# Optimization experiments

Hardware: AMD Instinct MI355X
Metric: run time of the kernel (lower is better)

The kernel has to match this reference:

```python
import jax, jax.numpy as jnp
import numpy as np
from jax import lax

B, A, SEQ, FIN = 512, 16, 50, 6
H, H2, T, G, S = 256, 128, 60, 64, 6
GR0, GR1 = -50.0, 50.0
CELL = (GR1 - GR0) / G
NTYPES, EMB = 10, 16
NENC, NL = 5, 2

def setup_inputs() -> dict:
    key = jax.random.key(0)
    ks = jax.random.split(key, 40)
    def rn(k, shape, scale=0.05):
        return (jax.random.normal(k, shape) * scale).astype(jnp.float32)
    history = jax.random.normal(ks[0], (B, A, SEQ, FIN), dtype=jnp.float32)
    types = jax.random.randint(ks[1], (B,), 0, NTYPES)
    history = history.at[:, 0, 0, 5].set(types.astype(jnp.float32))
    d = dict(history=history)
    d['emb'] = rn(ks[2], (NTYPES, EMB))
    d['fe_W1'] = rn(ks[3], (FIN + EMB, H)); d['fe_b1'] = jnp.zeros((H,), jnp.float32)
    d['fe_W2'] = rn(ks[4], (H, H));        d['fe_b2'] = jnp.zeros((H,), jnp.float32)
    d['enc_Wih'] = rn(ks[5], (NENC, NL, H, 3 * H))
    d['enc_Whh'] = rn(ks[6], (NENC, NL, H, 3 * H))
    d['enc_bih'] = rn(ks[7], (NENC, NL, 3 * H))
    d['enc_bhh'] = rn(ks[8], (NENC, NL, 3 * H))
    d['dec_Wih0'] = rn(ks[9], (2, 3 * H)); d['dec_Whh0'] = rn(ks[10], (H, 3 * H))
    d['dec_bih0'] = rn(ks[11], (3 * H));   d['dec_bhh0'] = rn(ks[12], (3 * H))
    d['dec_Wih1'] = rn(ks[13], (H, 3 * H)); d['dec_Whh1'] = rn(ks[14], (H, 3 * H))
    d['dec_bih1'] = rn(ks[15], (3 * H));    d['dec_bhh1'] = rn(ks[16], (3 * H))
    d['hg_W1'] = rn(ks[17], (H, H));   d['hg_b1'] = jnp.zeros((H,), jnp.float32)
    d['hg_W2'] = rn(ks[18], (H, H2));  d['hg_b2'] = jnp.zeros((H2,), jnp.float32)
    d['hg_W3'] = rn(ks[19], (H2, T * 2)); d['hg_b3'] = jnp.zeros((T * 2,), jnp.float32)
    d['ce_W1'] = rn(ks[20], (H, H2));  d['ce_b1'] = jnp.zeros((H2,), jnp.float32)
    d['ce_W2'] = rn(ks[21], (H2, T));  d['ce_b2'] = jnp.zeros((T,), jnp.float32)
    d['hp_W1'] = rn(ks[22], (H, H));   d['hp_b1'] = jnp.zeros((H,), jnp.float32)
    d['hp_W2'] = rn(ks[23], (H, G * G)); d['hp_b2'] = jnp.zeros((G * G,), jnp.float32)
    return d

def _gru_cell(xt, h, Wih, Whh, bih, bhh):
    # torch GRU gate order: r, z, n
    gi = xt @ Wih + bih
    gh = h @ Whh + bhh
    Hd = h.shape[-1]
    r = jax.nn.sigmoid(gi[:, :Hd] + gh[:, :Hd])
    z = jax.nn.sigmoid(gi[:, Hd:2 * Hd] + gh[:, Hd:2 * Hd])
    n = jnp.tanh(gi[:, 2 * Hd:] + r * gh[:, 2 * Hd:])
    return (1.0 - z) * n + z * h

def _forward(history, emb, fe_W1, fe_b1, fe_W2, fe_b2,
             enc_Wih, enc_Whh, enc_bih, enc_bhh,
             dec_Wih0, dec_Whh0, dec_bih0, dec_bhh0,
             dec_Wih1, dec_Whh1, dec_bih1, dec_bhh1,
             hg_W1, hg_b1, hg_W2, hg_b2, hg_W3, hg_b3,
             ce_W1, ce_b1, ce_W2, ce_b2, hp_W1, hp_b1, hp_W2, hp_b2):
    ego = history[:, 0]                                   # [B,SEQ,6]
    etype = jnp.clip(ego[:, 0, 5].astype(jnp.int32), 0, 9)
    # type -> encoder index (vehicle,pedestrian,cyclist,bus,default)
    eidx = jnp.array([0, 1, 4, 2, 3, 4, 4, 4, 4, 4], jnp.int32)[etype]
    te = emb[etype]                                       # [B,16]
    x_in = jnp.concatenate([ego, jnp.broadcast_to(te[:, None, :], (B, SEQ, EMB))], axis=-1)
    feat = jax.nn.relu(x_in @ fe_W1 + fe_b1) @ fe_W2 + fe_b2  # [B,SEQ,H]

    # 2-layer GRU with per-example (type-gathered) weights
    x_cur = feat.transpose(1, 0, 2)                       # [SEQ,B,H]
    h_finals = []
    for l in range(NL):
        Wih = enc_Wih[eidx, l]; Whh = enc_Whh[eidx, l]    # [B,H,3H]
        bih = enc_bih[eidx, l]; bhh = enc_bhh[eidx, l]    # [B,3H]
        def step(h, xt, Wih=Wih, Whh=Whh, bih=bih, bhh=bhh):
            gi = jnp.einsum('bd,bdg->bg', xt, Wih) + bih
            gh = jnp.einsum('bh,bhg->bg', h, Whh) + bhh
            r = jax.nn.sigmoid(gi[:, :H] + gh[:, :H])
            z = jax.nn.sigmoid(gi[:, H:2 * H] + gh[:, H:2 * H])
            n = jnp.tanh(gi[:, 2 * H:] + r * gh[:, 2 * H:])
            hn = (1.0 - z) * n + z * h
            return hn, hn
        h_last, ys = lax.scan(step, jnp.zeros((B, H), feat.dtype), x_cur)
        x_cur = ys
        h_finals.append(h_last)
    enc_h0, enc_h1 = h_finals

    # decoder GRU, single timestep: x = last ego position
    x0 = ego[:, -1, :2]
    h0 = _gru_cell(x0, enc_h0, dec_Wih0, dec_Whh0, dec_bih0, dec_bhh0)
    h1 = _gru_cell(h0, enc_h1, dec_Wih1, dec_Whh1, dec_bih1, dec_bhh1)
    last_hidden = h1                                      # [B,H]

    traj = (jax.nn.relu(jax.nn.relu(last_hidden @ hg_W1 + hg_b1) @ hg_W2 + hg_b2) @ hg_W3 + hg_b3)
    traj = traj.reshape(B, T, 2)
    conf = jax.nn.relu(last_hidden @ ce_W1 + ce_b1) @ ce_W2 + ce_b2   # [B,T]

    key = jax.random.key(42)
    k_noise, k_samp = jax.random.split(key)
    noise = jax.random.normal(k_noise, (T, B, H), last_hidden.dtype)
    scale = (0.1 * jnp.arange(T, dtype=last_hidden.dtype) / T)[:, None, None]
    th = last_hidden[None] + noise * scale                # [T,B,H]
    logits = jax.nn.relu(th @ hp_W1 + hp_b1) @ hp_W2 + hp_b2  # [T,B,G*G]

    # vectorized multinomial over (samples, timesteps, batch)
    idx = jax.random.categorical(k_samp, logits, shape=(S - 1, T, B))  # int [S-1,T,B]
    x_idx = (idx % G).astype(jnp.float32)
    y_idx = (idx // G).astype(jnp.float32)
    pts = jnp.stack([GR0 + x_idx * CELL + CELL / 2,
                     GR0 + y_idx * CELL + CELL / 2], axis=-1)  # [S-1,T,B,2]
    pts = pts.transpose(2, 0, 1, 3)                       # [B,S-1,T,2]

    predictions = jnp.concatenate([traj[:, None], pts], axis=1)  # [B,S,T,2]
    decay = jnp.float32(0.9) ** jnp.arange(S, dtype=jnp.float32)
    confidences = conf.mean(axis=1)[:, None] * decay[None, :]    # [B,S]
    return predictions, confidences

def reference(history, emb, fe_W1, fe_b1, fe_W2, fe_b2,
              enc_Wih, enc_Whh, enc_bih, enc_bhh,
              dec_Wih0, dec_Whh0, dec_bih0, dec_bhh0,
              dec_Wih1, dec_Whh1, dec_bih1, dec_bhh1,
              hg_W1, hg_b1, hg_W2, hg_b2, hg_W3, hg_b3,
              ce_W1, ce_b1, ce_W2, ce_b2, hp_W1, hp_b1, hp_W2, hp_b2):
    return _forward(history, emb, fe_W1, fe_b1, fe_W2, fe_b2,
                    enc_Wih, enc_Whh, enc_bih, enc_bhh,
                    dec_Wih0, dec_Whh0, dec_bih0, dec_bhh0,
                    dec_Wih1, dec_Whh1, dec_bih1, dec_bhh1,
                    hg_W1, hg_b1, hg_W2, hg_b2, hg_W3, hg_b3,
                    ce_W1, ce_b1, ce_W2, ce_b2, hp_W1, hp_b1, hp_W2, hp_b2)
```

## Files before the change

### kernel.cpp

```cpp
#include <hip/hip_runtime.h>
#include <stdint.h>
#include <math.h>

#define JAX_PARTITIONABLE 1

#define B_ 512
#define SEQ_ 50
#define H_ 256
#define H2_ 128
#define T_ 60
#define S_ 6
#define EMB_ 16
#define NL_ 2
#define TG_ 768
#define CAT_ 4096
#define GUMBEL_N 629145600u
#define NOISE_N 7864320u

typedef float f32x2 __attribute__((ext_vector_type(2)));

#define PKFMA_LO(acc, w, h) \
  asm("v_pk_fma_f32 %0, %1, %2, %0 op_sel:[0,0,0] op_sel_hi:[1,0,1]" : "+v"(acc) : "v"(w), "v"(h))
#define PKFMA_HI(acc, w, h) \
  asm("v_pk_fma_f32 %0, %1, %2, %0 op_sel:[0,1,0] op_sel_hi:[1,1,1]" : "+v"(acc) : "v"(w), "v"(h))

__host__ __device__ inline uint32_t rotl32(uint32_t x, int r) {
#if defined(__HIP_DEVICE_COMPILE__)
  return __builtin_amdgcn_alignbit(x, x, 32 - r);
#else
  return (x << r) | (x >> (32 - r));
#endif
}

__host__ __device__ inline void tf2x32(uint32_t k0, uint32_t k1, uint32_t x0, uint32_t x1,
                                       uint32_t& o0, uint32_t& o1) {
  uint32_t ks2 = k0 ^ k1 ^ 0x1BD11BDAu;
  x0 += k0; x1 += k1;
#define TFR(r) do { x0 += x1; x1 = rotl32(x1, r); x1 ^= x0; } while (0)
  TFR(13); TFR(15); TFR(26); TFR(6);
  x0 += k1; x1 += ks2 + 1u;
  TFR(17); TFR(29); TFR(16); TFR(24);
  x0 += ks2; x1 += k0 + 2u;
  TFR(13); TFR(15); TFR(26); TFR(6);
  x0 += k0; x1 += k1 + 3u;
  TFR(17); TFR(29); TFR(16); TFR(24);
  x0 += k1; x1 += ks2 + 4u;
  TFR(13); TFR(15); TFR(26); TFR(6);
  x0 += ks2; x1 += k0 + 5u;
#undef TFR
  o0 = x0; o1 = x1;
}

__device__ inline uint32_t jax_bits(uint32_t k0, uint32_t k1, uint32_t i, uint32_t n) {
#if JAX_PARTITIONABLE
  (void)n;
  uint32_t a, b;
  tf2x32(k0, k1, 0u, i, a, b);
  return a ^ b;
#else
  uint32_t half = n >> 1;
  uint32_t lo = (i < half) ? i : (i - half);
  uint32_t a, b;
  tf2x32(k0, k1, lo, lo + half, a, b);
  return (i < half) ? a : b;
#endif
}

__device__ inline float bits_to_f01(uint32_t bits) {
  return __uint_as_float((bits >> 9) | 0x3f800000u) - 1.0f;
}

__device__ inline float erfinv_f(float x) {
  double xd = (double)x;
  float w = (float)(-log((1.0 - xd) * (1.0 + xd)));
  float p;
  if (w < 5.0f) {
    w = __fadd_rn(w, -2.5f);
    p = 2.81022636e-08f;
    p = __fadd_rn(3.43273939e-07f, __fmul_rn(p, w));
    p = __fadd_rn(-3.5233877e-06f, __fmul_rn(p, w));
    p = __fadd_rn(-4.39150654e-06f, __fmul_rn(p, w));
    p = __fadd_rn(0.00021858087f, __fmul_rn(p, w));
    p = __fadd_rn(-0.00125372503f, __fmul_rn(p, w));
    p = __fadd_rn(-0.00417768164f, __fmul_rn(p, w));
    p = __fadd_rn(0.246640727f, __fmul_rn(p, w));
    p = __fadd_rn(1.50140941f, __fmul_rn(p, w));
  } else {
    w = __fadd_rn(__fsqrt_rn(w), -3.0f);
    p = -0.000200214257f;
    p = __fadd_rn(0.000100950558f, __fmul_rn(p, w));
    p = __fadd_rn(0.00134934322f, __fmul_rn(p, w));
    p = __fadd_rn(-0.00367342844f, __fmul_rn(p, w));
    p = __fadd_rn(0.00573950773f, __fmul_rn(p, w));
    p = __fadd_rn(-0.0076224613f, __fmul_rn(p, w));
    p = __fadd_rn(0.00943887047f, __fmul_rn(p, w));
    p = __fadd_rn(1.00167406f, __fmul_rn(p, w));
    p = __fadd_rn(2.83297682f, __fmul_rn(p, w));
  }
  return __fmul_rn(p, x);
}

__device__ inline float gumbel_f32(uint32_t bits) {
  float f = bits_to_f01(bits);
  float u = fmaxf(f, 1.17549435e-38f);
  float l1 = logf(u);
  return -logf(-l1);
}

__device__ inline uint32_t orderkey(float s) {
  uint32_t sb = __float_as_uint(s);
  return (sb & 0x80000000u) ? ~sb : (sb | 0x80000000u);
}

__global__ __launch_bounds__(512) void k_init(const float* __restrict__ hist,
                                              float* __restrict__ x0buf, int* __restrict__ ip) {
  int b = threadIdx.x;
  if (b < B_) {
    float tv = hist[b * 4800 + 5];
    int et = (int)tv;
    et = et < 0 ? 0 : (et > 9 ? 9 : et);
    const int mp[10] = {0, 1, 4, 2, 3, 4, 4, 4, 4, 4};
    ip[b] = et;
    ip[512 + b] = mp[et];
    x0buf[b * 2 + 0] = hist[b * 4800 + 49 * 6 + 0];
    x0buf[b * 2 + 1] = hist[b * 4800 + 49 * 6 + 1];
  }
  __syncthreads();
  if (b == 0) {
    int cnt[5] = {0, 0, 0, 0, 0};
    for (int i = 0; i < B_; i++) cnt[ip[512 + i]]++;
    int off[6];
    off[0] = 0;
    for (int e = 0; e < 5; e++) off[e + 1] = off[e] + cnt[e];
    int pos[5];
    for (int e = 0; e < 5; e++) pos[e] = off[e];
    for (int i = 0; i < B_; i++) { int e = ip[512 + i]; ip[1024 + pos[e]++] = i; }
    int* tbl = ip + 1536;
    int nrt = 0;
    for (int e = 0; e < 5; e++) {
      int n = cnt[e];
      for (int s = 0; s < n; s += 16) {
        tbl[1 + nrt] = e;
        tbl[37 + nrt] = off[e] + s;
        tbl[73 + nrt] = (n - s) < 16 ? (n - s) : 16;
        nrt++;
      }
    }
    tbl[0] = nrt;
  }
}

__global__ void k_zero(uint32_t* p, int n) {
  int i = blockIdx.x * blockDim.x + threadIdx.x;
  if (i < n) p[i] = 0u;
}

__global__ __launch_bounds__(256) void k_pack(const float* __restrict__ Wih,
                                              const float* __restrict__ Whh,
                                              float4* __restrict__ wp) {
  int i = blockIdx.x * 256 + threadIdx.x;
  if (i >= 20 * 65536) return;
  int cl = i & 31;
  int k  = (i >> 5) & 255;
  int cg = (i >> 13) & 7;
  int em = i >> 16;
  int m = em & 1;
  int el = em >> 1;
  int c = cg * 32 + cl;
  const float* W = (m ? Whh : Wih) + (size_t)el * H_ * TG_;
  float4 v;
  v.x = W[k * TG_ + c];
  v.y = W[k * TG_ + H_ + c];
  v.z = W[k * TG_ + 2 * H_ + c];
  v.w = 0.0f;
  wp[i] = v;
}

__global__ __launch_bounds__(256) void k_feat(const float* __restrict__ hist, const float* __restrict__ emb,
    const float* __restrict__ W1, const float* __restrict__ b1,
    const float* __restrict__ W2, const float* __restrict__ b2,
    const int* __restrict__ ip, float* __restrict__ featbuf) {
  __shared__ float xs[16][22];
  __shared__ float t1[16][H_];
  int row0 = blockIdx.x * 16;
  int tid = threadIdx.x;
  for (int idx = tid; idx < 16 * 22; idx += 256) {
    int r = idx / 22, c = idx % 22;
    int g = row0 + r;
    int b = g / SEQ_, s = g % SEQ_;
    xs[r][c] = (c < 6) ? hist[b * 4800 + s * 6 + c] : emb[ip[b] * EMB_ + (c - 6)];
  }
  __syncthreads();
  int j = tid;
  {
    double acc[16];
    for (int r = 0; r < 16; r++) acc[r] = 0.0;
    for (int k = 0; k < 22; k++) {
      double w = (double)W1[k * H_ + j];
      for (int r = 0; r < 16; r++) acc[r] += (double)xs[r][k] * w;
    }
    double bb = (double)b1[j];
    for (int r = 0; r < 16; r++) t1[r][j] = fmaxf((float)(acc[r] + bb), 0.0f);
  }
  __syncthreads();
  {
    double acc[16];
    for (int r = 0; r < 16; r++) acc[r] = 0.0;
    for (int k = 0; k < H_; k++) {
      double w = (double)W2[k * H_ + j];
      for (int r = 0; r < 16; r++) acc[r] += (double)t1[r][k] * w;
    }
    double bb = (double)b2[j];
    for (int r = 0; r < 16; r++) {
      float v = (float)(acc[r] + bb);
      int g = row0 + r;
      int b = g / SEQ_, s = g % SEQ_;
      featbuf[(size_t)s * (B_ * H_) + (size_t)b * H_ + j] = v;
    }
  }
}

#define KS_STAGE(dst, src)                                             \
  for (int idx = tid; idx < 16 * 64; idx += 512) {                     \
    int r = idx >> 6, c4 = idx & 63;                                   \
    int rr = (r < nr) ? r : 0;                                         \
    int b = order[start + rr];                                         \
    if (c4 == 0) rowb[r] = b;                                          \
    *(float4*)&dst[r][c4 * 4] = *(const float4*)&src[b * H_ + c4 * 4]; \
  }

#define KS_LOOP(src)                                                        \
  for (int k = k0; k < k0 + 128; k += 4) {                                  \
    float4 w0 = wp[(k + 0) * 32], w1 = wp[(k + 1) * 32];                    \
    float4 w2 = wp[(k + 2) * 32], w3 = wp[(k + 3) * 32];                    \
    float4 xa = *(const float4*)&src[rs][k];                                \
    float4 xb = *(const float4*)&src[rs + 8][k];                            \
    a0 += (double)xa.x * (double)w0.x; a1 += (double)xb.x * (double)w0.x;   \
    z0 += (double)xa.x * (double)w0.y; z1 += (double)xb.x * (double)w0.y;   \
    n0 += (double)xa.x * (double)w0.z; n1 += (double)xb.x * (double)w0.z;   \
    a0 += (double)xa.y * (double)w1.x; a1 += (double)xb.y * (double)w1.x;   \
    z0 += (double)xa.y * (double)w1.y; z1 += (double)xb.y * (double)w1.y;   \
    n0 += (double)xa.y * (double)w1.z; n1 += (double)xb.y * (double)w1.z;   \
    a0 += (double)xa.z * (double)w2.x; a1 += (double)xb.z * (double)w2.x;   \
    z0 += (double)xa.z * (double)w2.y; z1 += (double)xb.z * (double)w2.y;   \
    n0 += (double)xa.z * (double)w2.z; n1 += (double)xb.z * (double)w2.z;   \
    a0 += (double)xa.w * (double)w3.x; a1 += (double)xb.w * (double)w3.x;   \
    z0 += (double)xa.w * (double)w3.y; z1 += (double)xb.w * (double)w3.y;   \
    n0 += (double)xa.w * (double)w3.z; n1 += (double)xb.w * (double)w3.z;   \
  }

__device__ __forceinline__ void gi_block_ks(float (*xs)[H_], int* rowb,
    double (*part)[32][6],
    int rt, int cg, int tid,
    const float* __restrict__ x, float* __restrict__ gi_out,
    const float4* __restrict__ wpack, const float* __restrict__ bih_base,
    int layer, const int* __restrict__ ip) {
  const int* tbl = ip + 1536;
  const int* order = ip + 1024;
  int nrt = tbl[0];
  if (rt >= nrt) return;
  int e = tbl[1 + rt];
  int start = tbl[37 + rt];
  int nr = tbl[73 + rt];
  KS_STAGE(xs, x)
  __syncthreads();
  int j = tid & 31, rs = (tid >> 5) & 7, kh = tid >> 8;
  int c = cg * 32 + j;
  int el = e * NL_ + layer;
  const float4* wp = wpack + (((size_t)(el * 2 + 0) * 8 + cg) * 256) * 32 + j;
  int k0 = kh * 128;
  double a0 = 0, a1 = 0, z0 = 0, z1 = 0, n0 = 0, n1 = 0;
  KS_LOOP(xs)
  if (kh) {
    double* pp = &part[rs][j][0];
    pp[0] = a0; pp[1] = a1; pp[2] = z0; pp[3] = z1; pp[4] = n0; pp[5] = n1;
  }
  __syncthreads();
  if (!kh) {
    const double* pp = &part[rs][j][0];
    a0 += pp[0]; a1 += pp[1]; z0 += pp[2]; z1 += pp[3]; n0 += pp[4]; n1 += pp[5];
    int cr = c, cz = H_ + c, cn = 2 * H_ + c;
    const float* bih = bih_base + (size_t)el * TG_;
    double br = (double)bih[cr], bz = (double)bih[cz], bn = (double)bih[cn];
    for (int p = 0; p < 2; p++) {
      int r = rs + 8 * p;
      if (r >= nr) continue;
      int b = rowb[r];
      gi_out[b * TG_ + cr] = (float)((p ? a1 : a0) + br);
      gi_out[b * TG_ + cz] = (float)((p ? z1 : z0) + bz);
      gi_out[b * TG_ + cn] = (float)((p ? n1 : n0) + bn);
    }
  }
}

__device__ __forceinline__ void step_block_ks(float (*hs)[H_], int* rowb,
    double (*part)[32][6],
    int rt, int cg, int tid,
    const float* __restrict__ gi_in, const float* __restrict__ hin,
    float* __restrict__ hout, float* __restrict__ ys,
    const float4* __restrict__ wpack, const float* __restrict__ bhh_base,
    int layer, const int* __restrict__ ip) {
  const int* tbl = ip + 1536;
  const int* order = ip + 1024;
  int nrt = tbl[0];
  if (rt >= nrt) return;
  int e = tbl[1 + rt];
  int start = tbl[37 + rt];
  int nr = tbl[73 + rt];
  KS_STAGE(hs, hin)
  __syncthreads();
  int j = tid & 31, rs = (tid >> 5) & 7, kh = tid >> 8;
  int c = cg * 32 + j;
  int el = e * NL_ + layer;
  const float4* wp = wpack + (((size_t)(el * 2 + 1) * 8 + cg) * 256) * 32 + j;
  int k0 = kh * 128;
  double a0 = 0, a1 = 0, z0 = 0, z1 = 0, n0 = 0, n1 = 0;
  KS_LOOP(hs)
  if (kh) {
    double* pp = &part[rs][j][0];
    pp[0] = a0; pp[1] = a1; pp[2] = z0; pp[3] = z1; pp[4] = n0; pp[5] = n1;
  }
  __syncthreads();
  if (!kh) {
    const double* pp = &part[rs][j][0];
    a0 += pp[0]; a1 += pp[1]; z0 += pp[2]; z1 += pp[3]; n0 += pp[4]; n1 += pp[5];
    int cr = c, cz = H_ + c, cn = 2 * H_ + c;
    const float* bhh = bhh_base + (size_t)el * TG_;
    double bhr = (double)bhh[cr], bhz = (double)bhh[cz], bhn = (double)bhh[cn];
    for (int p = 0; p < 2; p++) {
      int r = rs + 8 * p;
      if (r >= nr) continue;
      int b = rowb[r];
      double gir = (double)gi_in[b * TG_ + cr];
      double giz = (double)gi_in[b * TG_ + cz];
      double gin = (double)gi_in[b * TG_ + cn];
      double ghr = (p ? a1 : a0) + bhr;
      double ghz = (p ? z1 : z0) + bhz;
      double ghn = (p ? n1 : n0) + bhn;
      double rr = 1.0 / (1.0 + exp(-(gir + ghr)));
      double zz = 1.0 / (1.0 + exp(-(giz + ghz)));
      double nn = tanh(gin + rr * ghn);
      double hv = (double)hs[r][c];
      float hnew = (float)((1.0 - zz) * nn + zz * hv);
      hout[b * H_ + c] = hnew;
      if (ys) ys[b * H_ + c] = hnew;
    }
  }
}

__global__ __launch_bounds__(512) void k_pipe512(int d,
    const float* __restrict__ feat, float* __restrict__ ys0,
    float* __restrict__ gi0, float* __restrict__ gi1,
    float* __restrict__ h0A, float* __restrict__ h0B,
    float* __restrict__ h1A, float* __restrict__ h1B,
    const float4* __restrict__ wpack,
    const float* __restrict__ bih, const float* __restrict__ bhh,
    const int* __restrict__ ip) {
  __shared__ float sb[16][H_];
  __shared__ double part[8][32][6];
  __shared__ int rowb[16];
  int g = blockIdx.x;
  int grp = g / 288, bx = g % 288;
  int rt = bx >> 3, cg = bx & 7;
  int tid = threadIdx.x;
  if (grp == 0) {
    int t = d; if (t >= SEQ_) return;
    gi_block_ks(sb, rowb, part, rt, cg, tid, feat + (size_t)t * 131072,
                gi0 + (size_t)(t & 1) * 393216, wpack, bih, 0, ip);
  } else if (grp == 1) {
    int t = d - 1; if (t < 0 || t >= SEQ_) return;
    const float* hin = (t & 1) ? h0B : h0A;
    float* hout = (t & 1) ? h0A : h0B;
    step_block_ks(sb, rowb, part, rt, cg, tid, gi0 + (size_t)(t & 1) * 393216,
                  hin, hout, ys0 + (size_t)t * 131072, wpack, bhh, 0, ip);
  } else if (grp == 2) {
    int t = d - 2; if (t < 0 || t >= SEQ_) return;
    gi_block_ks(sb, rowb, part, rt, cg, tid, ys0 + (size_t)t * 131072,
                gi1 + (size_t)(t & 1) * 393216, wpack, bih, 1, ip);
  } else {
    int t = d - 3; if (t < 0 || t >= SEQ_) return;
    const float* hin = (t & 1) ? h1B : h1A;
    float* hout = (t & 1) ? h1A : h1B;
    step_block_ks(sb, rowb, part, rt, cg, tid, gi1 + (size_t)(t & 1) * 393216,
                  hin, hout, nullptr, wpack, bhh, 1, ip);
  }
}

__device__ __forceinline__ void gi_block_u(float (*xs)[H_], int* rowb,
    int rt, int cg, int tid,
    const float* __restrict__ x, float* __restrict__ gi_out,
    const float* __restrict__ Wih_base, const float* __restrict__ bih_base,
    int layer, const int* __restrict__ ip) {
  const int* tbl = ip + 1536;
  const int* order = ip + 1024;
  int nrt = tbl[0];
  if (rt >= nrt) return;
  int e = tbl[1 + rt];
  int start = tbl[37 + rt];
  int nr = tbl[73 + rt];
  for (int idx = tid; idx < 16 * H_; idx += 256) {
    int r = idx >> 8, k = idx & 255;
    int rr = (r < nr) ? r : 0;
    int b = order[start + rr];
    if (k == 0) rowb[r] = b;
    xs[r][k] = x[b * H_ + k];
  }
  __syncthreads();
  size_t woff = (size_t)(e * NL_ + layer);
  const float* Wih = Wih_base + woff * (size_t)H_ * TG_;
  const float* bih = bih_base + woff * TG_;
  int j = tid & 31, rs = tid >> 5;
  int c = cg * 32 + j;
  int cr = c, cz = H_ + c, cn = 2 * H_ + c;
  double ar0 = 0, ar1 = 0, az0 = 0, az1 = 0, an0 = 0, an1 = 0;
  for (int k = 0; k < H_; k++) {
    float wr = Wih[k * TG_ + cr], wz = Wih[k * TG_ + cz], wn = Wih[k * TG_ + cn];
    float x0 = xs[rs][k], x1 = xs[rs + 8][k];
    ar0 += (double)x0 * wr; ar1 += (double)x1 * wr;
    az0 += (double)x0 * wz; az1 += (double)x1 * wz;
    an0 += (double)x0 * wn; an1 += (double)x1 * wn;
  }
  double br = (double)bih[cr], bz = (double)bih[cz], bn = (double)bih[cn];
  for (int p = 0; p < 2; p++) {
    int r = rs + 8 * p;
    if (r >= nr) continue;
    int b = rowb[r];
    gi_out[b * TG_ + cr] = (float)((p ? ar1 : ar0) + br);
    gi_out[b * TG_ + cz] = (float)((p ? az1 : az0) + bz);
    gi_out[b * TG_ + cn] = (float)((p ? an1 : an0) + bn);
  }
}

__device__ __forceinline__ void step_block_u(float (*hs)[H_], int* rowb,
    int rt, int cg, int tid,
    const float* __restrict__ gi_in, const float* __restrict__ hin,
    float* __restrict__ hout, float* __restrict__ ys,
    const float* __restrict__ Whh_base, const float* __restrict__ bhh_base,
    int layer, const int* __restrict__ ip) {
  const int* tbl = ip + 1536;
  const int* order = ip + 1024;
  int nrt = tbl[0];
  if (rt >= nrt) return;
  int e = tbl[1 + rt];
  int start = tbl[37 + rt];
  int nr = tbl[73 + rt];
  for (int idx = tid; idx < 16 * H_; idx += 256) {
    int r = idx >> 8, k = idx & 255;
    int rr = (r < nr) ? r : 0;
    int b = order[start + rr];
    if (k == 0) rowb[r] = b;
    hs[r][k] = hin[b * H_ + k];
  }
  __syncthreads();
  size_t woff = (size_t)(e * NL_ + layer);
  const float* Whh = Whh_base + woff * (size_t)H_ * TG_;
  const float* bhh = bhh_base + woff * TG_;
  int j = tid & 31, rs = tid >> 5;
  int c = cg * 32 + j;
  int cr = c, cz = H_ + c, cn = 2 * H_ + c;
  double gr0 = 0, gr1 = 0, gz0 = 0, gz1 = 0, gn0 = 0, gn1 = 0;
  for (int k = 0; k < H_; k++) {
    float wr = Whh[k * TG_ + cr], wz = Whh[k * TG_ + cz], wn = Whh[k * TG_ + cn];
    float h0 = hs[rs][k], h1 = hs[rs + 8][k];
    gr0 += (double)h0 * wr; gr1 += (double)h1 * wr;
    gz0 += (double)h0 * wz; gz1 += (double)h1 * wz;
    gn0 += (double)h0 * wn; gn1 += (double)h1 * wn;
  }
  double bhr = (double)bhh[cr], bhz = (double)bhh[cz], bhn = (double)bhh[cn];
  for (int p = 0; p < 2; p++) {
    int r = rs + 8 * p;
    if (r >= nr) continue;
    int b = rowb[r];
    double gir = (double)gi_in[b * TG_ + cr];
    double giz = (double)gi_in[b * TG_ + cz];
    double gin = (double)gi_in[b * TG_ + cn];
    double ghr = (p ? gr1 : gr0) + bhr;
    double ghz = (p ? gz1 : gz0) + bhz;
    double ghn = (p ? gn1 : gn0) + bhn;
    double rr = 1.0 / (1.0 + exp(-(gir + ghr)));
    double zz = 1.0 / (1.0 + exp(-(giz + ghz)));
    double nn = tanh(gin + rr * ghn);
    double hv = (double)hs[r][c];
    float hnew = (float)((1.0 - zz) * nn + zz * hv);
    hout[b * H_ + c] = hnew;
    if (ys) ys[b * H_ + c] = hnew;
  }
}

__global__ __launch_bounds__(256) void k_pipeu(int d,
    const float* __restrict__ feat, float* __restrict__ ys0,
    float* __restrict__ gi0, float* __restrict__ gi1,
    float* __restrict__ h0A, float* __restrict__ h0B,
    float* __restrict__ h1A, float* __restrict__ h1B,
    const float* __restrict__ Wih, const float* __restrict__ Whh,
    const float* __restrict__ bih, const float* __restrict__ bhh,
    const int* __restrict__ ip) {
  __shared__ float sb[16][H_];
  __shared__ int rowb[16];
  int g = blockIdx.x;
  int grp = g / 288, bx = g % 288;
  int rt = bx >> 3, cg = bx & 7;
  int tid = threadIdx.x;
  if (grp == 0) {
    int t = d; if (t >= SEQ_) return;
    gi_block_u(sb, rowb, rt, cg, tid, feat + (size_t)t * 131072,
               gi0 + (size_t)(t & 1) * 393216, Wih, bih, 0, ip);
  } else if (grp == 1) {
    int t = d - 1; if (t < 0 || t >= SEQ_) return;
    const float* hin = (t & 1) ? h0B : h0A;
    float* hout = (t & 1) ? h0A : h0B;
    step_block_u(sb, rowb, rt, cg, tid, gi0 + (size_t)(t & 1) * 393216,
                 hin, hout, ys0 + (size_t)t * 131072, Whh, bhh, 0, ip);
  } else if (grp == 2) {
    int t = d - 2; if (t < 0 || t >= SEQ_) return;
    gi_block_u(sb, rowb, rt, cg, tid, ys0 + (size_t)t * 131072,
               gi1 + (size_t)(t & 1) * 393216, Wih, bih, 1, ip);
  } else {
    int t = d - 3; if (t < 0 || t >= SEQ_) return;
    const float* hin = (t & 1) ? h1B : h1A;
    float* hout = (t & 1) ? h1A : h1B;
    step_block_u(sb, rowb, rt, cg, tid, gi1 + (size_t)(t & 1) * 393216,
                 hin, hout, nullptr, Whh, bhh, 1, ip);
  }
}

template <int D1>
__global__ __launch_bounds__(256) void k_gru(
    const float* __restrict__ x, const float* __restrict__ hin,
    float* __restrict__ hout,
    const float* __restrict__ Wih, const float* __restrict__ Whh,
    const float* __restrict__ bih, const float* __restrict__ bhh) {
  __shared__ float xs[16][(D1 == 2) ? 2 : H_];
  __shared__ float hs[16][H_];
  int bx = blockIdx.x, by = blockIdx.y;
  int start = bx * 16;
  int tid = threadIdx.x;
  for (int idx = tid; idx < 16 * H_; idx += 256) {
    int r = idx >> 8, k = idx & 255;
    int b = start + r;
    hs[r][k] = hin[b * H_ + k];
    if (D1 == H_) xs[r][k] = x[b * H_ + k];
    else if (k < D1) xs[r][k] = x[b * D1 + k];
  }
  __syncthreads();
  int j = tid & 31, rs = tid >> 5;
  int hc = by * 32 + j;
  int cr = hc, cz = H_ + hc, cn = 2 * H_ + hc;
  double ra0 = 0, ra1 = 0, za0 = 0, za1 = 0, ni0 = 0, ni1 = 0, nh0 = 0, nh1 = 0;
  for (int k = 0; k < H_; k++) {
    float wrh = Whh[k * TG_ + cr], wzh = Whh[k * TG_ + cz], wnh = Whh[k * TG_ + cn];
    float h0v = hs[rs][k], h1v = hs[rs + 8][k];
    ra0 += (double)h0v * wrh; ra1 += (double)h1v * wrh;
    za0 += (double)h0v * wzh; za1 += (double)h1v * wzh;
    nh0 += (double)h0v * wnh; nh1 += (double)h1v * wnh;
    if (D1 == H_) {
      float wri = Wih[k * TG_ + cr], wzi = Wih[k * TG_ + cz], wni = Wih[k * TG_ + cn];
      float x0v = xs[rs][k], x1v = xs[rs + 8][k];
      ra0 += (double)x0v * wri; ra1 += (double)x1v * wri;
      za0 += (double)x0v * wzi; za1 += (double)x1v * wzi;
      ni0 += (double)x0v * wni; ni1 += (double)x1v * wni;
    }
  }
  if (D1 != H_) {
    for (int k = 0; k < D1; k++) {
      float wri = Wih[k * TG_ + cr], wzi = Wih[k * TG_ + cz], wni = Wih[k * TG_ + cn];
      float x0v = xs[rs][k], x1v = xs[rs + 8][k];
      ra0 += (double)x0v * wri; ra1 += (double)x1v * wri;
      za0 += (double)x0v * wzi; za1 += (double)x1v * wzi;
      ni0 += (double)x0v * wni; ni1 += (double)x1v * wni;
    }
  }
  double br_i = (double)bih[cr], bz_i = (double)bih[cz], bn_i = (double)bih[cn];
  double br_h = (double)bhh[cr], bz_h = (double)bhh[cz], bn_h = (double)bhh[cn];
  for (int p = 0; p < 2; p++) {
    int r = rs + 8 * p;
    double ra = p ? ra1 : ra0, za = p ? za1 : za0, ni = p ? ni1 : ni0, nh = p ? nh1 : nh0;
    double rr = 1.0 / (1.0 + exp(-(ra + br_i + br_h)));
    double zz = 1.0 / (1.0 + exp(-(za + bz_i + bz_h)));
    double nn = tanh((ni + bn_i) + rr * (nh + bn_h));
    double hv = (double)hs[r][hc];
    float hnew = (float)((1.0 - zz) * nn + zz * hv);
    hout[(start + r) * H_ + hc] = hnew;
  }
}

__global__ __launch_bounds__(256) void k_heads(const float* __restrict__ lh,
    const float* __restrict__ hgW1, const float* __restrict__ hgb1,
    const float* __restrict__ hgW2, const float* __restrict__ hgb2,
    const float* __restrict__ hgW3, const float* __restrict__ hgb3,
    const float* __restrict__ ceW1, const float* __restrict__ ceb1,
    const float* __restrict__ ceW2, const float* __restrict__ ceb2,
    float* __restrict__ out) {
  __shared__ float hsm[16][H_];
  __shared__ float t1[16][H_];
  __shared__ float t2[16][H2_];
  __shared__ float c2s[16][T_];
  int row0 = blockIdx.x * 16;
  int tid = threadIdx.x;
  for (int idx = tid; idx < 16 * H_; idx += 256) {
    int r = idx >> 8, k = idx & 255;
    hsm[r][k] = lh[(size_t)(row0 + r) * H_ + k];
  }
  __syncthreads();
  {
    int j = tid;
    for (int r = 0; r < 16; r++) {
      double a = 0;
      for (int k = 0; k < H_; k++) a += (double)hsm[r][k] * (double)hgW1[k * H_ + j];
      t1[r][j] = fmaxf((float)(a + (double)hgb1[j]), 0.0f);
    }
  }
  __syncthreads();
  if (tid < H2_) {
    int j = tid;
    for (int r = 0; r < 16; r++) {
      double a = 0;
      for (int k = 0; k < H_; k++) a += (double)t1[r][k] * (double)hgW2[k * H2_ + j];
      t2[r][j] = fmaxf((float)(a + (double)hgb2[j]), 0.0f);
    }
  }
  __syncthreads();
  if (tid < 2 * T_) {
    int j = tid;
    for (int r = 0; r < 16; r++) {
      double a = 0;
      for (int k = 0; k < H2_; k++) a += (double)t2[r][k] * (double)hgW3[k * (2 * T_) + j];
      float v = (float)(a + (double)hgb3[j]);
      int b = row0 + r;
      int t = j >> 1, c = j & 1;
      out[(((size_t)b * S_ + 0) * T_ + t) * 2 + c] = v;
    }
  }
  __syncthreads();
  if (tid < H2_) {
    int j = tid;
    for (int r = 0; r < 16; r++) {
      double a = 0;
      for (int k = 0; k < H_; k++) a += (double)hsm[r][k] * (double)ceW1[k * H2_ + j];
      t2[r][j] = fmaxf((float)(a + (double)ceb1[j]), 0.0f);
    }
  }
  __syncthreads();
  if (tid < T_) {
    int j = tid;
    for (int r = 0; r < 16; r++) {
      double a = 0;
      for (int k = 0; k < H2_; k++) a += (double)t2[r][k] * (double)ceW2[k * T_ + j];
      c2s[r][j] = (float)(a + (double)ceb2[j]);
    }
  }
  __syncthreads();
  if (tid < 16) {
    int r = tid;
    int b = row0 + r;
    double s = 0;
    for (int j = 0; j < T_; j++) s += (double)c2s[r][j];
    float m = (float)(s / 60.0);
    for (int sd = 0; sd < S_; sd++) {
      float d = (float)pow((double)0.9f, (double)sd);
      out[368640 + b * S_ + sd] = __fmul_rn(m, d);
    }
  }
}

__global__ __launch_bounds__(256) void k_hp1(const float* __restrict__ lh,
    const float* __restrict__ W1, const float* __restrict__ b1,
    float* __restrict__ h1buf, uint32_t nk0, uint32_t nk1) {
  __shared__ float th[16][H_];
  int row0 = blockIdx.x * 16;
  int tid = threadIdx.x;
  const float SQRT2F = 1.4142135623730951f;
  const float LO = -0x1.fffffep-1f;
  for (int idx = tid; idx < 16 * H_; idx += 256) {
    int r = idx >> 8, k = idx & 255;
    int g = row0 + r;
    int t = g / B_, b = g % B_;
    uint32_t i = ((uint32_t)t * B_ + (uint32_t)b) * H_ + (uint32_t)k;
    uint32_t bits = jax_bits(nk0, nk1, i, NOISE_N);
    float f = bits_to_f01(bits);
    float u = fmaxf(LO, __fadd_rn(__fmul_rn(f, 2.0f), LO));
    float nz = __fmul_rn(SQRT2F, erfinv_f(u));
    float sc = __fdiv_rn(__fmul_rn(0.1f, (float)t), 60.0f);
    th[r][k] = __fadd_rn(lh[(size_t)b * H_ + k], __fmul_rn(nz, sc));
  }
  __syncthreads();
  int j = tid;
  double acc[16];
  for (int r = 0; r < 16; r++) acc[r] = 0.0;
  for (int k = 0; k < H_; k++) {
    double w = (double)W1[k * H_ + j];
    for (int r = 0; r < 16; r++) acc[r] += (double)th[r][k] * w;
  }
  double bb = (double)b1[j];
  for (int r = 0; r < 16; r++)
    h1buf[(size_t)(row0 + r) * H_ + j] = fmaxf((float)(acc[r] + bb), 0.0f);
}

__global__ __launch_bounds__(256) void k_hp2(const float* __restrict__ h1buf,
    const float* __restrict__ W2, const float* __restrict__ b2,
    unsigned long long* __restrict__ samples, uint32_t sk0, uint32_t sk1) {
  __shared__ float h1[16][H_];
  int row0 = blockIdx.x * 16;
  int cat0 = blockIdx.y * 256;
  int tid = threadIdx.x;
  for (int idx = tid; idx < 16 * H_ / 4; idx += 256) {
    int r = idx >> 6, k4 = (idx & 63) << 2;
    *(float4*)&h1[r][k4] = *(const float4*)&h1buf[(size_t)(row0 + r) * H_ + k4];
  }
  __syncthreads();
  int wave = tid >> 6;
  int lane = tid & 63;
  int catA = cat0 + 4 * lane;
  int rbase = 4 * wave;

  f32x2 acc[4][2];
#pragma unroll
  for (int r = 0; r < 4; r++) { acc[r][0] = (f32x2)0.0f; acc[r][1] = (f32x2)0.0f; }
  const float* w2p = W2 + catA;
  for (int k = 0; k < H_; k += 4) {
    float4 hv[4];
    hv[0] = *(const float4*)&h1[rbase + 0][k];
    hv[1] = *(const float4*)&h1[rbase + 1][k];
    hv[2] = *(const float4*)&h1[rbase + 2][k];
    hv[3] = *(const float4*)&h1[rbase + 3][k];
    float4 wv[4];
#pragma unroll
    for (int kk = 0; kk < 4; kk++) wv[kk] = *(const float4*)&w2p[(size_t)(k + kk) * CAT_];
#pragma unroll
    for (int kk = 0; kk < 4; kk++) {
      f32x2 wlo; wlo.x = wv[kk].x; wlo.y = wv[kk].y;
      f32x2 whi; whi.x = wv[kk].z; whi.y = wv[kk].w;
#pragma unroll
      for (int r = 0; r < 4; r++) {
        f32x2 hp;
        if (kk & 2) { hp.x = (&hv[r].x)[2]; hp.y = (&hv[r].x)[3]; }
        else        { hp.x = (&hv[r].x)[0]; hp.y = (&hv[r].x)[1]; }
        if (kk & 1) { PKFMA_HI(acc[r][0], wlo, hp); PKFMA_HI(acc[r][1], whi, hp); }
        else        { PKFMA_LO(acc[r][0], wlo, hp); PKFMA_LO(acc[r][1], whi, hp); }
      }
    }
  }
  float lg[4][4];
  float4 b4 = *(const float4*)&b2[catA];
#pragma unroll
  for (int r = 0; r < 4; r++) {
    lg[r][0] = __fadd_rn(acc[r][0].x, b4.x);
    lg[r][1] = __fadd_rn(acc[r][0].y, b4.y);
    lg[r][2] = __fadd_rn(acc[r][1].x, b4.z);
    lg[r][3] = __fadd_rn(acc[r][1].y, b4.w);
  }

  int t = row0 / B_;
  int bbase = row0 % B_;
#pragma unroll
  for (int s = 0; s < S_ - 1; s++) {
#pragma unroll
    for (int q = 0; q < 4; q++) {
      int brow = bbase + rbase + q;
      uint32_t ibase = (((uint32_t)s * T_ + (uint32_t)t) * B_ + (uint32_t)brow) * CAT_ + (uint32_t)catA;
      float sc0 = __fadd_rn(gumbel_f32(jax_bits(sk0, sk1, ibase + 0u, GUMBEL_N)), lg[q][0]);
      float sc1 = __fadd_rn(gumbel_f32(jax_bits(sk0, sk1, ibase + 1u, GUMBEL_N)), lg[q][1]);
      float sc2 = __fadd_rn(gumbel_f32(jax_bits(sk0, sk1, ibase + 2u, GUMBEL_N)), lg[q][2]);
      float sc3 = __fadd_rn(gumbel_f32(jax_bits(sk0, sk1, ibase + 3u, GUMBEL_N)), lg[q][3]);
      float bs = sc0; int bc = catA;
      if (sc1 > bs) { bs = sc1; bc = catA + 1; }
      if (sc2 > bs) { bs = sc2; bc = catA + 2; }
      if (sc3 > bs) { bs = sc3; bc = catA + 3; }
      float mv = bs;
      for (int off = 1; off < 64; off <<= 1)
        mv = fmaxf(mv, __shfl_xor(mv, off, 64));
      unsigned long long mask = __ballot(bs == mv);
      int src = __ffsll(mask) - 1;
      int wcat = __shfl(bc, src, 64);
      if (lane == 0) {
        unsigned long long p =
            (((unsigned long long)orderkey(mv)) << 32) | (unsigned long long)(~(uint32_t)wcat);
        atomicMax(&samples[((size_t)s * T_ + t) * B_ + brow], p);
      }
    }
  }
}

__global__ void k_emit(const unsigned long long* __restrict__ samples, float* __restrict__ out) {
  int gid = blockIdx.x * blockDim.x + threadIdx.x;
  if (gid >= (S_ - 1) * T_ * B_) return;
  int b = gid % B_;
  int t = (gid / B_) % T_;
  int s = gid / (B_ * T_);
  unsigned long long v = samples[gid];
  uint32_t cat = ~(uint32_t)(v & 0xFFFFFFFFu);
  float xi = (float)(cat & 63u);
  float yi = (float)(cat >> 6);
  float px = -50.0f + xi * 1.5625f + 0.78125f;
  float py = -50.0f + yi * 1.5625f + 0.78125f;
  size_t o = (((size_t)b * S_ + (size_t)(s + 1)) * T_ + t) * 2;
  out[o] = px;
  out[o + 1] = py;
}

extern "C" void kernel_launch(void* const* d_in, const int* in_sizes, int n_in,
                              void* d_out, int out_size, void* d_ws, size_t ws_size,
                              hipStream_t stream) {
  (void)in_sizes; (void)n_in; (void)out_size;
  const float* hist   = (const float*)d_in[0];
  const float* emb    = (const float*)d_in[1];
  const float* feW1   = (const float*)d_in[2];
  const float* feb1   = (const float*)d_in[3];
  const float* feW2   = (const float*)d_in[4];
  const float* feb2   = (const float*)d_in[5];
  const float* encWih = (const float*)d_in[6];
  const float* encWhh = (const float*)d_in[7];
  const float* encbih = (const float*)d_in[8];
  const float* encbhh = (const float*)d_in[9];
  const float* dWih0  = (const float*)d_in[10];
  const float* dWhh0  = (const float*)d_in[11];
  const float* dbih0  = (const float*)d_in[12];
  const float* dbhh0  = (const float*)d_in[13];
  const float* dWih1  = (const float*)d_in[14];
  const float* dWhh1  = (const float*)d_in[15];
  const float* dbih1  = (const float*)d_in[16];
  const float* dbhh1  = (const float*)d_in[17];
  const float* hgW1   = (const float*)d_in[18];
  const float* hgb1   = (const float*)d_in[19];
  const float* hgW2   = (const float*)d_in[20];
  const float* hgb2   = (const float*)d_in[21];
  const float* hgW3   = (const float*)d_in[22];
  const float* hgb3   = (const float*)d_in[23];
  const float* ceW1   = (const float*)d_in[24];
  const float* ceb1   = (const float*)d_in[25];
  const float* ceW2   = (const float*)d_in[26];
  const float* ceb2   = (const float*)d_in[27];
  const float* hpW1   = (const float*)d_in[28];
  const float* hpb1   = (const float*)d_in[29];
  const float* hpW2   = (const float*)d_in[30];
  const float* hpb2   = (const float*)d_in[31];
  float* out = (float*)d_out;
  float* ws = (float*)d_ws;

  float* feat  = ws;
  float* ys0   = ws + 6553600;
  float* gi0   = ws + 13107200;
  float* gi1   = ws + 13893632;
  float* h0A   = ws + 14680064;
  float* h0B   = h0A + 131072;
  float* h1A   = h0B + 131072;
  float* h1B   = h1A + 131072;
  float* dech0 = h1B + 131072;
  float* lh    = dech0 + 131072;
  float* x0buf = lh + 131072;
  int*   ip    = (int*)(x0buf + 1024);
  unsigned long long* samples =
      (unsigned long long*)(((uintptr_t)(ip + 2048) + 255) & ~(uintptr_t)255);
  float* h1hp  = ws;

  size_t samples_end = (size_t)((char*)(samples + 307200) - (char*)ws);
  size_t wpack_off = (samples_end + 255) & ~(size_t)255;
  float4* wpack = (float4*)((char*)ws + wpack_off);
  bool packed = (wpack_off + (size_t)20 * 65536 * 16) <= ws_size;

  uint32_t kn0, kn1, ks0, ks1;
#if JAX_PARTITIONABLE
  tf2x32(0u, 42u, 0u, 0u, kn0, kn1);
  tf2x32(0u, 42u, 0u, 1u, ks0, ks1);
#else
  { uint32_t a0, a1, b0, b1;
    tf2x32(0u, 42u, 0u, 2u, a0, a1);
    tf2x32(0u, 42u, 1u, 3u, b0, b1);
    kn0 = a0; kn1 = b0; ks0 = a1; ks1 = b1; }
#endif

  k_init<<<dim3(1), dim3(512), 0, stream>>>(hist, x0buf, ip);
  k_zero<<<dim3((524288 + 255) / 256), dim3(256), 0, stream>>>((uint32_t*)h0A, 524288);
  k_zero<<<dim3((307200 + 255) / 256), dim3(256), 0, stream>>>((uint32_t*)samples, 307200);
  if (packed)
    k_pack<<<dim3(5120), dim3(256), 0, stream>>>(encWih, encWhh, wpack);
  k_feat<<<dim3(1600), dim3(256), 0, stream>>>(hist, emb, feW1, feb1, feW2, feb2, ip, feat);

  for (int d = 0; d < SEQ_ + 3; d++) {
    if (packed)
      k_pipe512<<<dim3(1152), dim3(512), 0, stream>>>(d,
          feat, ys0, gi0, gi1, h0A, h0B, h1A, h1B,
          wpack, encbih, encbhh, ip);
    else
      k_pipeu<<<dim3(1152), dim3(256), 0, stream>>>(d,
          feat, ys0, gi0, gi1, h0A, h0B, h1A, h1B,
          encWih, encWhh, encbih, encbhh, ip);
  }

  k_gru<2><<<dim3(32, 8), dim3(256), 0, stream>>>(
      x0buf, h0A, dech0, dWih0, dWhh0, dbih0, dbhh0);
  k_gru<H_><<<dim3(32, 8), dim3(256), 0, stream>>>(
      dech0, h1A, lh, dWih1, dWhh1, dbih1, dbhh1);

  k_heads<<<dim3(32), dim3(256), 0, stream>>>(lh, hgW1, hgb1, hgW2, hgb2, hgW3, hgb3,
                                              ceW1, ceb1, ceW2, ceb2, out);
  k_hp1<<<dim3(1920), dim3(256), 0, stream>>>(lh, hpW1, hpb1, h1hp, kn0, kn1);
  k_hp2<<<dim3(1920, 16), dim3(256), 0, stream>>>(h1hp, hpW2, hpb2, samples, ks0, ks1);
  k_emit<<<dim3(600), dim3(256), 0, stream>>>(samples, out);
}
```

Baseline: 5.633 ms.

## Use 32-row batch tiles without split-K in encoder GRU pipeline kernel

The encoder GRU pipeline now groups batch rows per encoder into tiles of 32 instead of 16. It drops the two-way K split and its shared-memory double reduction, so each thread covers four rows over the full K range with 8-way unrolled weight loads. This doubles weight reuse per packed-weight load and shrinks the grid from 1152 blocks of 512 threads to 640 blocks of 256, cutting redundant weight traffic and a sync. In exchange each thread carries a longer serial FP64 chain, and fewer waves are in flight, which may hurt latency hiding.

New measurement: 5.500 ms. -2.4%, faster.

```diff
diff --git a/kernel.cpp b/kernel.cpp
--- a/kernel.cpp
+++ b/kernel.cpp
@@ -147,6 +147,18 @@
       }
     }
     tbl[0] = nrt;
+    int* t32 = ip + 1664;
+    int n32 = 0;
+    for (int e = 0; e < 5; e++) {
+      int n = cnt[e];
+      for (int s = 0; s < n; s += 32) {
+        t32[1 + n32] = e;
+        t32[21 + n32] = off[e] + s;
+        t32[41 + n32] = (n - s) < 32 ? (n - s) : 32;
+        n32++;
+      }
+    }
+    t32[0] = n32;
   }
 }
 
@@ -220,135 +232,138 @@
   }
 }
 
-#define KS_STAGE(dst, src)                                             \
-  for (int idx = tid; idx < 16 * 64; idx += 512) {                     \
-    int r = idx >> 6, c4 = idx & 63;                                   \
-    int rr = (r < nr) ? r : 0;                                         \
-    int b = order[start + rr];                                         \
-    if (c4 == 0) rowb[r] = b;                                          \
-    *(float4*)&dst[r][c4 * 4] = *(const float4*)&src[b * H_ + c4 * 4]; \
-  }
-
-#define KS_LOOP(src)                                                        \
-  for (int k = k0; k < k0 + 128; k += 4) {                                  \
-    float4 w0 = wp[(k + 0) * 32], w1 = wp[(k + 1) * 32];                    \
-    float4 w2 = wp[(k + 2) * 32], w3 = wp[(k + 3) * 32];                    \
-    float4 xa = *(const float4*)&src[rs][k];                                \
-    float4 xb = *(const float4*)&src[rs + 8][k];                            \
-    a0 += (double)xa.x * (double)w0.x; a1 += (double)xb.x * (double)w0.x;   \
-    z0 += (double)xa.x * (double)w0.y; z1 += (double)xb.x * (double)w0.y;   \
-    n0 += (double)xa.x * (double)w0.z; n1 += (double)xb.x * (double)w0.z;   \
-    a0 += (double)xa.y * (double)w1.x; a1 += (double)xb.y * (double)w1.x;   \
-    z0 += (double)xa.y * (double)w1.y; z1 += (double)xb.y * (double)w1.y;   \
-    n0 += (double)xa.y * (double)w1.z; n1 += (double)xb.y * (double)w1.z;   \
-    a0 += (double)xa.z * (double)w2.x; a1 += (double)xb.z * (double)w2.x;   \
-    z0 += (double)xa.z * (double)w2.y; z1 += (double)xb.z * (double)w2.y;   \
-    n0 += (double)xa.z * (double)w2.z; n1 += (double)xb.z * (double)w2.z;   \
-    a0 += (double)xa.w * (double)w3.x; a1 += (double)xb.w * (double)w3.x;   \
-    z0 += (double)xa.w * (double)w3.y; z1 += (double)xb.w * (double)w3.y;   \
-    n0 += (double)xa.w * (double)w3.z; n1 += (double)xb.w * (double)w3.z;   \
-  }
-
-__device__ __forceinline__ void gi_block_ks(float (*xs)[H_], int* rowb,
-    double (*part)[32][6],
+__device__ __forceinline__ void gi_block_32(float (*xs)[H_], int* rowb,
     int rt, int cg, int tid,
     const float* __restrict__ x, float* __restrict__ gi_out,
     const float4* __restrict__ wpack, const float* __restrict__ bih_base,
     int layer, const int* __restrict__ ip) {
-  const int* tbl = ip + 1536;
+  const int* t32 = ip + 1664;
   const int* order = ip + 1024;
-  int nrt = tbl[0];
+  int nrt = t32[0];
   if (rt >= nrt) return;
-  int e = tbl[1 + rt];
-  int start = tbl[37 + rt];
-  int nr = tbl[73 + rt];
-  KS_STAGE(xs, x)
-  __syncthreads();
-  int j = tid & 31, rs = (tid >> 5) & 7, kh = tid >> 8;
+  int e = t32[1 + rt];
+  int start = t32[21 + rt];
+  int nr = t32[41 + rt];
+  for (int idx = tid; idx < 32 * 64; idx += 256) {
+    int r = idx >> 6, c4 = idx & 63;
+    int rr = (r < nr) ? r : 0;
+    int b = order[start + rr];
+    if (c4 == 0) rowb[r] = b;
+    *(float4*)&xs[r][c4 * 4] = *(const float4*)&x[b * H_ + c4 * 4];
+  }
+  __syncthreads();
+  int j = tid & 31, rs = tid >> 5;
   int c = cg * 32 + j;
   int el = e * NL_ + layer;
   const float4* wp = wpack + (((size_t)(el * 2 + 0) * 8 + cg) * 256) * 32 + j;
-  int k0 = kh * 128;
-  double a0 = 0, a1 = 0, z0 = 0, z1 = 0, n0 = 0, n1 = 0;
-  KS_LOOP(xs)
-  if (kh) {
-    double* pp = &part[rs][j][0];
-    pp[0] = a0; pp[1] = a1; pp[2] = z0; pp[3] = z1; pp[4] = n0; pp[5] = n1;
-  }
-  __syncthreads();
-  if (!kh) {
-    const double* pp = &part[rs][j][0];
-    a0 += pp[0]; a1 += pp[1]; z0 += pp[2]; z1 += pp[3]; n0 += pp[4]; n1 += pp[5];
-    int cr = c, cz = H_ + c, cn = 2 * H_ + c;
-    const float* bih = bih_base + (size_t)el * TG_;
-    double br = (double)bih[cr], bz = (double)bih[cz], bn = (double)bih[cn];
-    for (int p = 0; p < 2; p++) {
-      int r = rs + 8 * p;
-      if (r >= nr) continue;
-      int b = rowb[r];
-      gi_out[b * TG_ + cr] = (float)((p ? a1 : a0) + br);
-      gi_out[b * TG_ + cz] = (float)((p ? z1 : z0) + bz);
-      gi_out[b * TG_ + cn] = (float)((p ? n1 : n0) + bn);
-    }
-  }
-}
-
-__device__ __forceinline__ void step_block_ks(float (*hs)[H_], int* rowb,
-    double (*part)[32][6],
+  double a[4] = {0, 0, 0, 0}, z[4] = {0, 0, 0, 0}, n[4] = {0, 0, 0, 0};
+  for (int k = 0; k < H_; k += 8) {
+    float4 w[8];
+#pragma unroll
+    for (int kk = 0; kk < 8; kk++) w[kk] = wp[(k + kk) * 32];
+    float4 xlo[4], xhi[4];
+#pragma unroll
+    for (int q = 0; q < 4; q++) {
+      xlo[q] = *(const float4*)&xs[rs + 8 * q][k];
+      xhi[q] = *(const float4*)&xs[rs + 8 * q][k + 4];
+    }
+#pragma unroll
+    for (int kk = 0; kk < 8; kk++) {
+#pragma unroll
+      for (int q = 0; q < 4; q++) {
+        float xv = (kk < 4) ? (&xlo[q].x)[kk] : (&xhi[q].x)[kk - 4];
+        a[q] += (double)xv * (double)w[kk].x;
+        z[q] += (double)xv * (double)w[kk].y;
+        n[q] += (double)xv * (double)w[kk].z;
+      }
+    }
+  }
+  int cr = c, cz = H_ + c, cn = 2 * H_ + c;
+  const float* bih = bih_base + (size_t)el * TG_;
+  double br = (double)bih[cr], bz = (double)bih[cz], bn = (double)bih[cn];
+#pragma unroll
+  for (int q = 0; q < 4; q++) {
+    int r = rs + 8 * q;
+    if (r >= nr) continue;
+    int b = rowb[r];
+    gi_out[b * TG_ + cr] = (float)(a[q] + br);
+    gi_out[b * TG_ + cz] = (float)(z[q] + bz);
+    gi_out[b * TG_ + cn] = (float)(n[q] + bn);
+  }
+}
+
+__device__ __forceinline__ void step_block_32(float (*hs)[H_], int* rowb,
     int rt, int cg, int tid,
     const float* __restrict__ gi_in, const float* __restrict__ hin,
     float* __restrict__ hout, float* __restrict__ ys,
     const float4* __restrict__ wpack, const float* __restrict__ bhh_base,
     int layer, const int* __restrict__ ip) {
-  const int* tbl = ip + 1536;
+  const int* t32 = ip + 1664;
   const int* order = ip + 1024;
-  int nrt = tbl[0];
+  int nrt = t32[0];
   if (rt >= nrt) return;
-  int e = tbl[1 + rt];
-  int start = tbl[37 + rt];
-  int nr = tbl[73 + rt];
-  KS_STAGE(hs, hin)
-  __syncthreads();
-  int j = tid & 31, rs = (tid >> 5) & 7, kh = tid >> 8;
+  int e = t32[1 + rt];
+  int start = t32[21 + rt];
+  int nr = t32[41 + rt];
+  for (int idx = tid; idx < 32 * 64; idx += 256) {
+    int r = idx >> 6, c4 = idx & 63;
+    int rr = (r < nr) ? r : 0;
+    int b = order[start + rr];
+    if (c4 == 0) rowb[r] = b;
+    *(float4*)&hs[r][c4 * 4] = *(const float4*)&hin[b * H_ + c4 * 4];
+  }
+  __syncthreads();
+  int j = tid & 31, rs = tid >> 5;
   int c = cg * 32 + j;
   int el = e * NL_ + layer;
   const float4* wp = wpack + (((size_t)(el * 2 + 1) * 8 + cg) * 256) * 32 + j;
-  int k0 = kh * 128;
-  double a0 = 0, a1 = 0, z0 = 0, z1 = 0, n0 = 0, n1 = 0;
-  KS_LOOP(hs)
-  if (kh) {
-    double* pp = &part[rs][j][0];
-    pp[0] = a0; pp[1] = a1; pp[2] = z0; pp[3] = z1; pp[4] = n0; pp[5] = n1;
-  }
-  __syncthreads();
-  if (!kh) {
-    const double* pp = &part[rs][j][0];
-    a0 += pp[0]; a1 += pp[1]; z0 += pp[2]; z1 += pp[3]; n0 += pp[4]; n1 += pp[5];
-    int cr = c, cz = H_ + c, cn = 2 * H_ + c;
-    const float* bhh = bhh_base + (size_t)el * TG_;
-    double bhr = (double)bhh[cr], bhz = (double)bhh[cz], bhn = (double)bhh[cn];
-    for (int p = 0; p < 2; p++) {
-      int r = rs + 8 * p;
-      if (r >= nr) continue;
-      int b = rowb[r];
-      double gir = (double)gi_in[b * TG_ + cr];
-      double giz = (double)gi_in[b * TG_ + cz];
-      double gin = (double)gi_in[b * TG_ + cn];
-      double ghr = (p ? a1 : a0) + bhr;
-      double ghz = (p ? z1 : z0) + bhz;
-      double ghn = (p ? n1 : n0) + bhn;
-      double rr = 1.0 / (1.0 + exp(-(gir + ghr)));
-      double zz = 1.0 / (1.0 + exp(-(giz + ghz)));
-      double nn = tanh(gin + rr * ghn);
-      double hv = (double)hs[r][c];
-      float hnew = (float)((1.0 - zz) * nn + zz * hv);
-      hout[b * H_ + c] = hnew;
-      if (ys) ys[b * H_ + c] = hnew;
-    }
-  }
-}
-
-__global__ __launch_bounds__(512) void k_pipe512(int d,
+  double a[4] = {0, 0, 0, 0}, z[4] = {0, 0, 0, 0}, n[4] = {0, 0, 0, 0};
+  for (int k = 0; k < H_; k += 8) {
+    float4 w[8];
+#pragma unroll
+    for (int kk = 0; kk < 8; kk++) w[kk] = wp[(k + kk) * 32];
+    float4 hlo[4], hhi[4];
+#pragma unroll
+    for (int q = 0; q < 4; q++) {
+      hlo[q] = *(const float4*)&hs[rs + 8 * q][k];
+      hhi[q] = *(const float4*)&hs[rs + 8 * q][k + 4];
+    }
+#pragma unroll
+    for (int kk = 0; kk < 8; kk++) {
+#pragma unroll
+      for (int q = 0; q < 4; q++) {
+        float hv = (kk < 4) ? (&hlo[q].x)[kk] : (&hhi[q].x)[kk - 4];
+        a[q] += (double)hv * (double)w[kk].x;
+        z[q] += (double)hv * (double)w[kk].y;
+        n[q] += (double)hv * (double)w[kk].z;
+      }
+    }
+  }
+  int cr = c, cz = H_ + c, cn = 2 * H_ + c;
+  const float* bhh = bhh_base + (size_t)el * TG_;
+  double bhr = (double)bhh[cr], bhz = (double)bhh[cz], bhn = (double)bhh[cn];
+#pragma unroll
+  for (int q = 0; q < 4; q++) {
+    int r = rs + 8 * q;
+    if (r >= nr) continue;
+    int b = rowb[r];
+    double gir = (double)gi_in[b * TG_ + cr];
+    double giz = (double)gi_in[b * TG_ + cz];
+    double gin = (double)gi_in[b * TG_ + cn];
+    double ghr = a[q] + bhr;
+    double ghz = z[q] + bhz;
+    double ghn = n[q] + bhn;
+    double rr = 1.0 / (1.0 + exp(-(gir + ghr)));
+    double zz = 1.0 / (1.0 + exp(-(giz + ghz)));
+    double nn = tanh(gin + rr * ghn);
+    double hv = (double)hs[r][c];
+    float hnew = (float)((1.0 - zz) * nn + zz * hv);
+    hout[b * H_ + c] = hnew;
+    if (ys) ys[b * H_ + c] = hnew;
+  }
+}
+
+__global__ __launch_bounds__(256) void k_pipe32(int d,
     const float* __restrict__ feat, float* __restrict__ ys0,
     float* __restrict__ gi0, float* __restrict__ gi1,
     float* __restrict__ h0A, float* __restrict__ h0B,
@@ -356,33 +371,38 @@
     const float4* __restrict__ wpack,
     const float* __restrict__ bih, const float* __restrict__ bhh,
     const int* __restrict__ ip) {
-  __shared__ float sb[16][H_];
-  __shared__ double part[8][32][6];
-  __shared__ int rowb[16];
+  __shared__ float sb[32][H_];
+  __shared__ int rowb[32];
   int g = blockIdx.x;
-  int grp = g / 288, bx = g % 288;
+  int grp = g / 160, bx = g % 160;
   int rt = bx >> 3, cg = bx & 7;
   int tid = threadIdx.x;
   if (grp == 0) {
-    int t = d; if (t >= SEQ_) return;
-    gi_block_ks(sb, rowb, part, rt, cg, tid, feat + (size_t)t * 131072,
-                gi0 + (size_t)(t & 1) * 393216, wpack, bih, 0, ip);
+    int t = d;
+    if (t < SEQ_)
+      gi_block_32(sb, rowb, rt, cg, tid, feat + (size_t)t * 131072,
+                  gi0 + (size_t)(t & 1) * 393216, wpack, bih, 0, ip);
   } else if (grp == 1) {
-    int t = d - 1; if (t < 0 || t >= SEQ_) return;
-    const float* hin = (t & 1) ? h0B : h0A;
-    float* hout = (t & 1) ? h0A : h0B;
-    step_block_ks(sb, rowb, part, rt, cg, tid, gi0 + (size_t)(t & 1) * 393216,
-                  hin, hout, ys0 + (size_t)t * 131072, wpack, bhh, 0, ip);
+    int t = d - 1;
+    if (t >= 0 && t < SEQ_) {
+      const float* hin = (t & 1) ? h0B : h0A;
+      float* hout = (t & 1) ? h0A : h0B;
+      step_block_32(sb, rowb, rt, cg, tid, gi0 + (size_t)(t & 1) * 393216,
+                    hin, hout, ys0 + (size_t)t * 131072, wpack, bhh, 0, ip);
+    }
   } else if (grp == 2) {
-    int t = d - 2; if (t < 0 || t >= SEQ_) return;
-    gi_block_ks(sb, rowb, part, rt, cg, tid, ys0 + (size_t)t * 131072,
-                gi1 + (size_t)(t & 1) * 393216, wpack, bih, 1, ip);
+    int t = d - 2;
+    if (t >= 0 && t < SEQ_)
+      gi_block_32(sb, rowb, rt, cg, tid, ys0 + (size_t)t * 131072,
+                  gi1 + (size_t)(t & 1) * 393216, wpack, bih, 1, ip);
   } else {
-    int t = d - 3; if (t < 0 || t >= SEQ_) return;
-    const float* hin = (t & 1) ? h1B : h1A;
-    float* hout = (t & 1) ? h1A : h1B;
-    step_block_ks(sb, rowb, part, rt, cg, tid, gi1 + (size_t)(t & 1) * 393216,
-                  hin, hout, nullptr, wpack, bhh, 1, ip);
+    int t = d - 3;
+    if (t >= 0 && t < SEQ_) {
+      const float* hin = (t & 1) ? h1B : h1A;
+      float* hout = (t & 1) ? h1A : h1B;
+      step_block_32(sb, rowb, rt, cg, tid, gi1 + (size_t)(t & 1) * 393216,
+                    hin, hout, nullptr, wpack, bhh, 1, ip);
+    }
   }
 }
 
@@ -876,12 +896,13 @@
     k_pack<<<dim3(5120), dim3(256), 0, stream>>>(encWih, encWhh, wpack);
   k_feat<<<dim3(1600), dim3(256), 0, stream>>>(hist, emb, feW1, feb1, feW2, feb2, ip, feat);
 
-  for (int d = 0; d < SEQ_ + 3; d++) {
-    if (packed)
-      k_pipe512<<<dim3(1152), dim3(512), 0, stream>>>(d,
+  if (packed) {
+    for (int d = 0; d < SEQ_ + 3; d++)
+      k_pipe32<<<dim3(640), dim3(256), 0, stream>>>(d,
           feat, ys0, gi0, gi1, h0A, h0B, h1A, h1B,
           wpack, encbih, encbhh, ip);
-    else
+  } else {
+    for (int d = 0; d < SEQ_ + 3; d++)
       k_pipeu<<<dim3(1152), dim3(256), 0, stream>>>(d,
           feat, ys0, gi0, gi1, h0A, h0B, h1A, h1B,
           encWih, encWhh, encbih, encbhh, ip);
```
